# Performance work log

Hardware: AMD Instinct MI355X
Metric: run time of the kernel (lower is better)

Reference implementation:

```python
import jax, jax.numpy as jnp
import numpy as np

B, C_IN, H, W = 8, 32, 64, 64
C = 64  # num_channels


def setup_inputs() -> dict:
    key = jax.random.key(0)
    ks = jax.random.split(key, 9)
    s_in = 1.0 / np.sqrt(C_IN)
    s_c = 1.0 / np.sqrt(C)
    return {
        "x": jax.random.normal(ks[0], (B, C_IN, H, W), dtype=jnp.float32),
        "wq": jax.random.uniform(ks[1], (C, C_IN), jnp.float32, -s_in, s_in),
        "bq": jax.random.uniform(ks[2], (C,), jnp.float32, -s_in, s_in),
        "wk": jax.random.uniform(ks[3], (C, C_IN), jnp.float32, -s_in, s_in),
        "bk": jax.random.uniform(ks[4], (C,), jnp.float32, -s_in, s_in),
        "wv": jax.random.uniform(ks[5], (C, C_IN), jnp.float32, -s_in, s_in),
        "bv": jax.random.uniform(ks[6], (C,), jnp.float32, -s_in, s_in),
        "wo": jax.random.uniform(ks[7], (C_IN, C), jnp.float32, -s_c, s_c),
        "bo": jax.random.uniform(ks[8], (C_IN,), jnp.float32, -s_c, s_c),
    }


def reference(x, wq, bq, wk, bk, wv, bv, wo, bo):
    b, c_in, h, w = x.shape
    n = h * w
    # 1x1 convs == per-pixel linear projections; produce (B, N, C) directly
    q = (jnp.einsum('bchw,oc->bhwo', x, wq) + bq).reshape(b, n, -1)
    k = (jnp.einsum('bchw,oc->bhwo', x, wk) + bk).reshape(b, n, -1)
    v = (jnp.einsum('bchw,oc->bhwo', x, wv) + bv).reshape(b, n, -1)
    # unscaled attention over spatial positions (no 1/sqrt(d) in original)
    scores = jnp.einsum('bnc,bmc->bnm', q, k)  # (B, N, N)
    attn = jax.nn.softmax(scores, axis=-1)
    out = jnp.einsum('bnm,bmc->bnc', attn, v)  # (B, N, C)
    out = out.reshape(b, h, w, -1)
    out = jnp.einsum('bhwc,oc->bohw', out, wo) + bo[None, :, None, None]
    return out + x
```

## Files before the change

kernel.cpp:

```cpp
#include <hip/hip_runtime.h>
#include <hip/hip_bf16.h>

#define CIN    32
#define NPIX   4096
#define DIM    64
#define LOG2E  1.4426950408889634f

#if __has_builtin(__builtin_amdgcn_exp2f)
#define EXP2(x) __builtin_amdgcn_exp2f(x)
#else
#define EXP2(x) exp2f(x)
#endif

typedef float  f32x4  __attribute__((ext_vector_type(4)));
typedef float  f32x16 __attribute__((ext_vector_type(16)));
typedef short  s16x8  __attribute__((ext_vector_type(8)));

#define ZERO16 {0.f,0.f,0.f,0.f,0.f,0.f,0.f,0.f,0.f,0.f,0.f,0.f,0.f,0.f,0.f,0.f}

__device__ __forceinline__ f32x16 mfma32(s16x8 a, s16x8 b, f32x16 c) {
    return __builtin_amdgcn_mfma_f32_32x32x16_bf16(a, b, c, 0, 0, 0);
}


__global__ __launch_bounds__(256) void qkv_proj(
    const float* __restrict__ x,
    const float* __restrict__ wq, const float* __restrict__ bq,
    const float* __restrict__ wk, const float* __restrict__ bk,
    const float* __restrict__ wv, const float* __restrict__ bv,
    __hip_bfloat16* __restrict__ qb, __hip_bfloat16* __restrict__ kb,
    __hip_bfloat16* __restrict__ vb)
{
    __shared__ float Xs[CIN][64];
    __shared__ float wT[3][CIN][DIM];

    const int tid = threadIdx.x;
    const int b   = blockIdx.y;
    const int bx  = blockIdx.x;
    const int n0  = bx * 64;

    for (int i = tid; i < 3 * CIN * DIM; i += 256) {
        int m = i >> 11, r = i & 2047, c = r >> 6, o = r & 63;
        const float* wsrc = (m == 0) ? wq : (m == 1) ? wk : wv;
        float wv0 = wsrc[o * CIN + c];
        wT[m][c][o] = (m == 0) ? wv0 * LOG2E : wv0;
    }
    for (int i = tid * 4; i < CIN * 64; i += 1024) {
        int c = i >> 6, p = i & 63;
        *(f32x4*)&Xs[c][p] = *(const f32x4*)&x[((size_t)b * CIN + c) * NPIX + n0 + p];
    }
    __syncthreads();

    const int w    = tid >> 6;
    const int lane = tid & 63;
    const int l16  = lane >> 2;
    const int quad = lane & 3;

    const int T  = bx * 4 + w;
    const int px = T * 16 + l16;

    float aq[2][8], ak[2][8];
    #pragma unroll
    for (int kb2 = 0; kb2 < 2; kb2++) {
        f32x4 bq0 = *(const f32x4*)&bq[kb2 * 32 + quad * 8];
        f32x4 bq1 = *(const f32x4*)&bq[kb2 * 32 + quad * 8 + 4];
        f32x4 bk0 = *(const f32x4*)&bk[kb2 * 32 + quad * 8];
        f32x4 bk1 = *(const f32x4*)&bk[kb2 * 32 + quad * 8 + 4];
        #pragma unroll
        for (int j = 0; j < 4; j++) {
            aq[kb2][j] = bq0[j] * LOG2E; aq[kb2][j + 4] = bq1[j] * LOG2E;
            ak[kb2][j] = bk0[j];         ak[kb2][j + 4] = bk1[j];
        }
    }
    #pragma unroll 8
    for (int c = 0; c < CIN; c++) {
        const float xc = Xs[c][w * 16 + l16];
        #pragma unroll
        for (int kb2 = 0; kb2 < 2; kb2++) {
            f32x4 q0 = *(const f32x4*)&wT[0][c][kb2 * 32 + quad * 8];
            f32x4 q1 = *(const f32x4*)&wT[0][c][kb2 * 32 + quad * 8 + 4];
            f32x4 k0 = *(const f32x4*)&wT[1][c][kb2 * 32 + quad * 8];
            f32x4 k1 = *(const f32x4*)&wT[1][c][kb2 * 32 + quad * 8 + 4];
            #pragma unroll
            for (int j = 0; j < 4; j++) {
                aq[kb2][j]     += xc * q0[j];
                aq[kb2][j + 4] += xc * q1[j];
                ak[kb2][j]     += xc * k0[j];
                ak[kb2][j + 4] += xc * k1[j];
            }
        }
    }
    {
        const int s   = px >> 5;
        const int key = px & 31;
        #pragma unroll
        for (int kb2 = 0; kb2 < 2; kb2++) {
            union { s16x8 v; __hip_bfloat16 h[8]; } pq, pk;
            #pragma unroll
            for (int j = 0; j < 8; j++) {
                pq.h[j] = __float2bfloat16(aq[kb2][j]);
                pk.h[j] = __float2bfloat16(ak[kb2][j]);
            }
            *(s16x8*)(qb + ((size_t)b * NPIX + px) * DIM + kb2 * 32 + quad * 8) = pq.v;
            const int kt = kb2 * 2 + (quad >> 1);
            const int h  = quad & 1;
            const size_t koff = (size_t)b * 262144
                + ((size_t)(s * 4 + kt) * 64 + h * 32 + key) * 8;
            *(s16x8*)(kb + koff) = pk.v;
        }
    }

    const int ch = w * 16 + l16;
    float av[2][8];
    {
        const float bvc = bv[ch];
        #pragma unroll
        for (int kh = 0; kh < 2; kh++)
            #pragma unroll
            for (int j = 0; j < 8; j++) av[kh][j] = bvc;
    }
    #pragma unroll 8
    for (int c = 0; c < CIN; c++) {
        const float wvc = wT[2][c][ch];
        f32x4 x0 = *(const f32x4*)&Xs[c][quad * 8];
        f32x4 x1 = *(const f32x4*)&Xs[c][quad * 8 + 4];
        f32x4 x2 = *(const f32x4*)&Xs[c][32 + quad * 8];
        f32x4 x3 = *(const f32x4*)&Xs[c][32 + quad * 8 + 4];
        #pragma unroll
        for (int j = 0; j < 4; j++) {
            av[0][j]     += x0[j] * wvc;
            av[0][j + 4] += x1[j] * wvc;
            av[1][j]     += x2[j] * wvc;
            av[1][j + 4] += x3[j] * wvc;
        }
    }
    #pragma unroll
    for (int kh = 0; kh < 2; kh++) {
        const int s = bx * 2 + kh;
        #pragma unroll
        for (int h = 0; h < 2; h++) {
            union { unsigned long long u; __hip_bfloat16 hh[4]; } pv;
            #pragma unroll
            for (int j = 0; j < 4; j++) pv.hh[j] = __float2bfloat16(av[kh][h * 4 + j]);
            const size_t voff = (size_t)b * 262144
                + (size_t)(s * 4 + (ch >> 5) * 2 + (quad >> 1)) * 512
                + (size_t)(h * 32 + (ch & 31)) * 8
                + 4 * (quad & 1);
            *(unsigned long long*)(vb + voff) = pv.u;
        }
    }
}

__global__ __launch_bounds__(512, 4) void attn_fused(
    const __hip_bfloat16* __restrict__ qb,
    const __hip_bfloat16* __restrict__ kbf,
    const __hip_bfloat16* __restrict__ vbf,
    const float* __restrict__ wo, const float* __restrict__ bo,
    const float* __restrict__ x, float* __restrict__ y)
{
    __shared__ __align__(16) char sm[2][8][4096];
    __shared__ float LRED2[4][32];

    float (*REDx)[64][33] = (float (*)[64][33])&sm[0][0][0];

    const int tid  = threadIdx.x;
    const int w    = tid >> 6;
    const int g    = w >> 1;
    const int h    = w & 1;
    const int lane = tid & 63;
    const int q    = lane & 31;
    const int hl   = lane >> 5;
    const int b    = blockIdx.x;
    const int row0 = blockIdx.y * 128 + g * 32;

    s16x8 qf[4];
    #pragma unroll
    for (int kt = 0; kt < 4; kt++)
        qf[kt] = *(const s16x8*)(qb + ((size_t)b * NPIX + row0 + q) * DIM
                                 + kt * 16 + hl * 8);

    f32x16 o0 = ZERO16, o1 = ZERO16;
    float lsacc = 0.f;

    const char* stbase = ((w >> 2) ? (const char*)vbf : (const char*)kbf)
                       + (size_t)b * 524288
                       + (size_t)((w >> 1) & 1) * 262144
                       + (size_t)(w & 1) * 4096
                       + (size_t)lane * 16;
    char* std0 = &sm[0][w][lane * 16];
    char* std1 = &sm[1][w][lane * 16];

    #pragma unroll
    for (int i = 0; i < 4; i++)
        *(f32x4*)(std0 + i * 1024) = *(const f32x4*)(stbase + i * 1024);
    __syncthreads();

    int cur = 0;
    for (int p = 0; p < 32; ++p) {
        const char* K0 = sm[cur][h * 2 + 0];
        const char* K1 = sm[cur][h * 2 + 1];
        s16x8 kf0[4], kf1[4];
        #pragma unroll
        for (int i = 0; i < 4; i++) {
            kf0[i] = *(const s16x8*)(K0 + i * 1024 + lane * 16);
            kf1[i] = *(const s16x8*)(K1 + i * 1024 + lane * 16);
        }

        __builtin_amdgcn_s_setprio(1);
        f32x16 s0 = ZERO16, s1 = ZERO16;
        s0 = mfma32(kf0[0], qf[0], s0);
        s1 = mfma32(kf1[0], qf[0], s1);
        s0 = mfma32(kf0[1], qf[1], s0);
        s1 = mfma32(kf1[1], qf[1], s1);
        s0 = mfma32(kf0[2], qf[2], s0);
        s1 = mfma32(kf1[2], qf[2], s1);
        s0 = mfma32(kf0[3], qf[3], s0);
        s1 = mfma32(kf1[3], qf[3], s1);
        __builtin_amdgcn_s_setprio(0);

        const size_t srcoff = (size_t)((p < 31) ? p + 1 : 31) * 8192;
        f32x4 r0 = *(const f32x4*)(stbase + srcoff);
        f32x4 r1 = *(const f32x4*)(stbase + srcoff + 1024);
        f32x4 r2 = *(const f32x4*)(stbase + srcoff + 2048);
        f32x4 r3 = *(const f32x4*)(stbase + srcoff + 3072);

        union { s16x8 v; __hip_bfloat16 h8[8]; } p00, p01, p10, p11;
        #pragma unroll
        for (int r = 0; r < 16; r++) { s0[r] = EXP2(s0[r]); lsacc += s0[r]; }
        #pragma unroll
        for (int j = 0; j < 8; j++) {
            p00.h8[j] = __float2bfloat16(s0[j]);
            p01.h8[j] = __float2bfloat16(s0[8 + j]);
        }
        #pragma unroll
        for (int r = 0; r < 16; r++) { s1[r] = EXP2(s1[r]); lsacc += s1[r]; }
        #pragma unroll
        for (int j = 0; j < 8; j++) {
            p10.h8[j] = __float2bfloat16(s1[j]);
            p11.h8[j] = __float2bfloat16(s1[8 + j]);
        }

        const char* V0 = sm[cur][4 + h * 2 + 0];
        const char* V1 = sm[cur][4 + h * 2 + 1];
        s16x8 vv0[4], vv1[4];
        #pragma unroll
        for (int i = 0; i < 4; i++) {
            vv0[i] = *(const s16x8*)(V0 + i * 1024 + lane * 16);
            vv1[i] = *(const s16x8*)(V1 + i * 1024 + lane * 16);
        }

        __builtin_amdgcn_s_setprio(1);
        o0 = mfma32(vv0[0], p00.v, o0);
        o1 = mfma32(vv0[2], p00.v, o1);
        o0 = mfma32(vv0[1], p01.v, o0);
        o1 = mfma32(vv0[3], p01.v, o1);
        o0 = mfma32(vv1[0], p10.v, o0);
        o1 = mfma32(vv1[2], p10.v, o1);
        o0 = mfma32(vv1[1], p11.v, o0);
        o1 = mfma32(vv1[3], p11.v, o1);
        __builtin_amdgcn_s_setprio(0);

        char* dst = cur ? std0 : std1;
        *(f32x4*)(dst)        = r0;
        *(f32x4*)(dst + 1024) = r1;
        *(f32x4*)(dst + 2048) = r2;
        *(f32x4*)(dst + 3072) = r3;
        __syncthreads();
        cur ^= 1;
    }

    lsacc += __shfl_xor(lsacc, 32, 64);

    if (h == 1) {
        #pragma unroll
        for (int i = 0; i < 16; i++) {
            const int rr = (i & 3) + 8 * (i >> 2) + 4 * hl;
            REDx[g][rr][q]      = o0[i];
            REDx[g][32 + rr][q] = o1[i];
        }
        if (hl == 0) LRED2[g][q] = lsacc;
    }
    __syncthreads();

    if (h == 0) {
        const float lsum = lsacc + LRED2[g][q];
        #pragma unroll
        for (int i = 0; i < 16; i++) {
            const int rr = (i & 3) + 8 * (i >> 2) + 4 * hl;
            o0[i] += REDx[g][rr][q];
            o1[i] += REDx[g][32 + rr][q];
        }
        const float inv = 1.0f / lsum;

        s16x8 pbo[4];
        #pragma unroll
        for (int gg = 0; gg < 4; gg++) {
            union { s16x8 v; __hip_bfloat16 h8[8]; } pk;
            #pragma unroll
            for (int j = 0; j < 8; j++) {
                const float vv = (gg < 2) ? o0[(gg & 1) * 8 + j] : o1[(gg & 1) * 8 + j];
                pk.h8[j] = __float2bfloat16(vv * inv);
            }
            pbo[gg] = pk.v;
        }

        s16x8 aw[4];
        #pragma unroll
        for (int gg = 0; gg < 4; gg++) {
            f32x4 w0 = *(const f32x4*)(wo + (size_t)q * DIM + gg * 16 + hl * 4);
            f32x4 w1 = *(const f32x4*)(wo + (size_t)q * DIM + gg * 16 + 8 + hl * 4);
            union { s16x8 v; __hip_bfloat16 h8[8]; } wf;
            #pragma unroll
            for (int j = 0; j < 4; j++) {
                wf.h8[j]     = __float2bfloat16(w0[j]);
                wf.h8[4 + j] = __float2bfloat16(w1[j]);
            }
            aw[gg] = wf.v;
        }

        f32x16 d = ZERO16;
        #pragma unroll
        for (int gg = 0; gg < 4; gg++)
            d = mfma32(aw[gg], pbo[gg], d);

        #pragma unroll
        for (int i = 0; i < 16; i++) {
            const int out = (i & 3) + 8 * (i >> 2) + 4 * hl;
            const int row = row0 + q;
            const size_t xi = ((size_t)b * CIN + out) * NPIX + row;
            y[xi] = d[i] + bo[out] + x[xi];
        }
    }
}

extern "C" void kernel_launch(void* const* d_in, const int* in_sizes, int n_in,
                              void* d_out, int out_size, void* d_ws, size_t ws_size,
                              hipStream_t stream)
{
    const float* x  = (const float*)d_in[0];
    const float* wq = (const float*)d_in[1];
    const float* bq = (const float*)d_in[2];
    const float* wk = (const float*)d_in[3];
    const float* bk = (const float*)d_in[4];
    const float* wv = (const float*)d_in[5];
    const float* bv = (const float*)d_in[6];
    const float* wo = (const float*)d_in[7];
    const float* bo = (const float*)d_in[8];
    float* y = (float*)d_out;

    char* ws = (char*)d_ws;
    __hip_bfloat16* qb = (__hip_bfloat16*)(ws);
    __hip_bfloat16* kb = (__hip_bfloat16*)(ws + (4u << 20));
    __hip_bfloat16* vb = (__hip_bfloat16*)(ws + (8u << 20));

    qkv_proj<<<dim3(64, 8), dim3(256), 0, stream>>>(x, wq, bq, wk, bk, wv, bv, qb, kb, vb);
    attn_fused<<<dim3(8, 32), dim3(512), 0, stream>>>(qb, kb, vb, wo, bo, x, y);
}
```

Measured before the change: 129.3 us.

## Split key range four ways per query tile and double the grid

Each block now covers 64 query rows instead of 128, and the grid doubles to 64 row-blocks per batch. Eight waves form two query groups times four key-quarter splits, and each wave handles one key/value tile per step instead of two, so per-wave work per iteration halves. The partial outputs and row sums from three of the splits are reduced through shared memory into the first split. This trades more blocks and parallelism for twice the total K/V streaming and a larger final reduction. The QK product also changes from a plain bf16 sum to a split sA+sB sum, and that pairing relies on the staged data layout.

```diff
diff --git a/kernel.cpp b/kernel.cpp
--- a/kernel.cpp
+++ b/kernel.cpp
@@ -159,19 +159,19 @@
     const float* __restrict__ x, float* __restrict__ y)
 {
     __shared__ __align__(16) char sm[2][8][4096];
-    __shared__ float LRED2[4][32];
-
-    float (*REDx)[64][33] = (float (*)[64][33])&sm[0][0][0];
+    __shared__ float LRED2[3][2][32];
+
+    float (*REDq)[2][64][33] = (float (*)[2][64][33])&sm[0][0][0];
 
     const int tid  = threadIdx.x;
     const int w    = tid >> 6;
-    const int g    = w >> 1;
-    const int h    = w & 1;
+    const int g    = w >> 2;
+    const int kq   = w & 3;
     const int lane = tid & 63;
     const int q    = lane & 31;
     const int hl   = lane >> 5;
     const int b    = blockIdx.x;
-    const int row0 = blockIdx.y * 128 + g * 32;
+    const int row0 = blockIdx.y * 64 + g * 32;
 
     s16x8 qf[4];
     #pragma unroll
@@ -184,8 +184,7 @@
 
     const char* stbase = ((w >> 2) ? (const char*)vbf : (const char*)kbf)
                        + (size_t)b * 524288
-                       + (size_t)((w >> 1) & 1) * 262144
-                       + (size_t)(w & 1) * 4096
+                       + (size_t)(w & 3) * 131072
                        + (size_t)lane * 16;
     char* std0 = &sm[0][w][lane * 16];
     char* std1 = &sm[1][w][lane * 16];
@@ -197,67 +196,47 @@
 
     int cur = 0;
     for (int p = 0; p < 32; ++p) {
-        const char* K0 = sm[cur][h * 2 + 0];
-        const char* K1 = sm[cur][h * 2 + 1];
-        s16x8 kf0[4], kf1[4];
-        #pragma unroll
-        for (int i = 0; i < 4; i++) {
-            kf0[i] = *(const s16x8*)(K0 + i * 1024 + lane * 16);
-            kf1[i] = *(const s16x8*)(K1 + i * 1024 + lane * 16);
-        }
-
-        __builtin_amdgcn_s_setprio(1);
-        f32x16 s0 = ZERO16, s1 = ZERO16;
-        s0 = mfma32(kf0[0], qf[0], s0);
-        s1 = mfma32(kf1[0], qf[0], s1);
-        s0 = mfma32(kf0[1], qf[1], s0);
-        s1 = mfma32(kf1[1], qf[1], s1);
-        s0 = mfma32(kf0[2], qf[2], s0);
-        s1 = mfma32(kf1[2], qf[2], s1);
-        s0 = mfma32(kf0[3], qf[3], s0);
-        s1 = mfma32(kf1[3], qf[3], s1);
-        __builtin_amdgcn_s_setprio(0);
-
-        const size_t srcoff = (size_t)((p < 31) ? p + 1 : 31) * 8192;
+        const char* Kl = sm[cur][kq];
+        s16x8 kf[4];
+        #pragma unroll
+        for (int i = 0; i < 4; i++)
+            kf[i] = *(const s16x8*)(Kl + i * 1024 + lane * 16);
+
+        const size_t srcoff = (size_t)((p < 31) ? p + 1 : 31) * 4096;
         f32x4 r0 = *(const f32x4*)(stbase + srcoff);
         f32x4 r1 = *(const f32x4*)(stbase + srcoff + 1024);
         f32x4 r2 = *(const f32x4*)(stbase + srcoff + 2048);
         f32x4 r3 = *(const f32x4*)(stbase + srcoff + 3072);
 
-        union { s16x8 v; __hip_bfloat16 h8[8]; } p00, p01, p10, p11;
-        #pragma unroll
-        for (int r = 0; r < 16; r++) { s0[r] = EXP2(s0[r]); lsacc += s0[r]; }
+        __builtin_amdgcn_s_setprio(1);
+        f32x16 sA = ZERO16, sB = ZERO16;
+        sA = mfma32(kf[0], qf[0], sA);
+        sB = mfma32(kf[2], qf[2], sB);
+        sA = mfma32(kf[1], qf[1], sA);
+        sB = mfma32(kf[3], qf[3], sB);
+        __builtin_amdgcn_s_setprio(0);
+
+        union { s16x8 v; __hip_bfloat16 h8[8]; } p0, p1;
         #pragma unroll
         for (int j = 0; j < 8; j++) {
-            p00.h8[j] = __float2bfloat16(s0[j]);
-            p01.h8[j] = __float2bfloat16(s0[8 + j]);
-        }
-        #pragma unroll
-        for (int r = 0; r < 16; r++) { s1[r] = EXP2(s1[r]); lsacc += s1[r]; }
-        #pragma unroll
-        for (int j = 0; j < 8; j++) {
-            p10.h8[j] = __float2bfloat16(s1[j]);
-            p11.h8[j] = __float2bfloat16(s1[8 + j]);
-        }
-
-        const char* V0 = sm[cur][4 + h * 2 + 0];
-        const char* V1 = sm[cur][4 + h * 2 + 1];
-        s16x8 vv0[4], vv1[4];
-        #pragma unroll
-        for (int i = 0; i < 4; i++) {
-            vv0[i] = *(const s16x8*)(V0 + i * 1024 + lane * 16);
-            vv1[i] = *(const s16x8*)(V1 + i * 1024 + lane * 16);
-        }
+            float e0 = EXP2(sA[j] + sB[j]);
+            float e1 = EXP2(sA[8 + j] + sB[8 + j]);
+            lsacc += e0 + e1;
+            p0.h8[j] = __float2bfloat16(e0);
+            p1.h8[j] = __float2bfloat16(e1);
+        }
+
+        const char* Vl = sm[cur][4 + kq];
+        s16x8 vv[4];
+        #pragma unroll
+        for (int i = 0; i < 4; i++)
+            vv[i] = *(const s16x8*)(Vl + i * 1024 + lane * 16);
 
         __builtin_amdgcn_s_setprio(1);
-        o0 = mfma32(vv0[0], p00.v, o0);
-        o1 = mfma32(vv0[2], p00.v, o1);
-        o0 = mfma32(vv0[1], p01.v, o0);
-        o1 = mfma32(vv0[3], p01.v, o1);
-        o0 = mfma32(vv1[0], p10.v, o0);
-        o1 = mfma32(vv1[2], p10.v, o1);
-        o0 = mfma32(vv1[1], p11.v, o0);
-        o1 = mfma32(vv1[3], p11.v, o1);
+        o0 = mfma32(vv[0], p0.v, o0);
+        o1 = mfma32(vv[2], p0.v, o1);
+        o0 = mfma32(vv[1], p1.v, o0);
+        o1 = mfma32(vv[3], p1.v, o1);
         __builtin_amdgcn_s_setprio(0);
 
         char* dst = cur ? std0 : std1;
@@ -271,26 +250,29 @@
 
     lsacc += __shfl_xor(lsacc, 32, 64);
 
-    if (h == 1) {
+    if (kq != 0) {
         #pragma unroll
         for (int i = 0; i < 16; i++) {
             const int rr = (i & 3) + 8 * (i >> 2) + 4 * hl;
-            REDx[g][rr][q]      = o0[i];
-            REDx[g][32 + rr][q] = o1[i];
-        }
-        if (hl == 0) LRED2[g][q] = lsacc;
+            REDq[kq - 1][g][rr][q]      = o0[i];
+            REDq[kq - 1][g][32 + rr][q] = o1[i];
+        }
+        if (hl == 0) LRED2[kq - 1][g][q] = lsacc;
     }
     __syncthreads();
 
-    if (h == 0) {
-        const float lsum = lsacc + LRED2[g][q];
-        #pragma unroll
-        for (int i = 0; i < 16; i++) {
-            const int rr = (i & 3) + 8 * (i >> 2) + 4 * hl;
-            o0[i] += REDx[g][rr][q];
-            o1[i] += REDx[g][32 + rr][q];
-        }
-        const float inv = 1.0f / lsum;
+    if (kq == 0) {
+        #pragma unroll
+        for (int sl = 0; sl < 3; sl++) {
+            lsacc += LRED2[sl][g][q];
+            #pragma unroll
+            for (int i = 0; i < 16; i++) {
+                const int rr = (i & 3) + 8 * (i >> 2) + 4 * hl;
+                o0[i] += REDq[sl][g][rr][q];
+                o1[i] += REDq[sl][g][32 + rr][q];
+            }
+        }
+        const float inv = 1.0f / lsacc;
 
         s16x8 pbo[4];
         #pragma unroll
@@ -298,8 +280,8 @@
             union { s16x8 v; __hip_bfloat16 h8[8]; } pk;
             #pragma unroll
             for (int j = 0; j < 8; j++) {
-                const float vv = (gg < 2) ? o0[(gg & 1) * 8 + j] : o1[(gg & 1) * 8 + j];
-                pk.h8[j] = __float2bfloat16(vv * inv);
+                const float vv2 = (gg < 2) ? o0[(gg & 1) * 8 + j] : o1[(gg & 1) * 8 + j];
+                pk.h8[j] = __float2bfloat16(vv2 * inv);
             }
             pbo[gg] = pk.v;
         }
@@ -354,5 +336,5 @@
     __hip_bfloat16* vb = (__hip_bfloat16*)(ws + (8u << 20));
 
     qkv_proj<<<dim3(64, 8), dim3(256), 0, stream>>>(x, wq, bq, wk, bk, wv, bv, qb, kb, vb);
-    attn_fused<<<dim3(8, 32), dim3(512), 0, stream>>>(qb, kb, vb, wo, bo, x, y);
+    attn_fused<<<dim3(8, 64), dim3(512), 0, stream>>>(qb, kb, vb, wo, bo, x, y);
 }
```

After: 134.8 us. 1.04x slower.
